# Optimization experiments

Measured on AMD Instinct MI355X. Metric: run time of the kernel, lower is better.

Reference implementation:

```python
import jax, jax.numpy as jnp
import numpy as np

B, S, D, H, DK = 32, 1024, 256, 8, 32
MASK_VALUE = -1e-30  # note: NOT -inf; masked scores become ~0 pre-softmax, faithful to source


def setup_inputs() -> dict:
    key = jax.random.key(0)
    ks = jax.random.split(key, 7)
    query = jax.random.normal(ks[0], (B, S, D), dtype=jnp.float32)
    key_t = jax.random.normal(ks[1], (B, S, D), dtype=jnp.float32)
    value = jax.random.normal(ks[2], (B, S, D), dtype=jnp.float32)
    # binary observation mask over key positions
    mask = (jax.random.uniform(ks[3], (B, S)) > 0.5).astype(jnp.float32)
    glorot = jax.nn.initializers.glorot_uniform(in_axis=1, out_axis=2)
    Wq = glorot(ks[4], (H, D, DK), jnp.float32)
    Wk = glorot(ks[5], (H, D, DK), jnp.float32)
    Wv = glorot(ks[6], (H, D, DK), jnp.float32)
    return {"query": query, "key": key_t, "value": value, "mask": mask,
            "Wq": Wq, "Wk": Wk, "Wv": Wv}


def reference(query, key, value, mask, Wq, Wk, Wv):
    # per-head projections, vectorized over heads: [B,S,D] x [H,D,DK] -> [B,H,S,DK]
    q = jnp.einsum('bsd,hdk->bhsk', query, Wq)
    k = jnp.einsum('bsd,hdk->bhsk', key, Wk)
    v = jnp.einsum('bsd,hdk->bhsk', value, Wv)
    # raw scores (no 1/sqrt(dk) scaling in source): [B,H,Sq,Sk]
    A = jnp.einsum('bhqk,bhsk->bhqs', q, k)
    m = mask[:, None, None, :]  # [B,1,1,Sk]
    A = m * A + (1.0 - m) * MASK_VALUE  # multiplicative mask, NOT additive
    A = jax.nn.softmax(A, axis=-1)
    out = jnp.einsum('bhqs,bhsk->bhqk', A, v)  # [B,H,Sq,DK]
    # concat heads along last dim, matching torch.cat order
    return out.transpose(0, 2, 1, 3).reshape(B, S, H * DK)
```

## Files before the change

### kernel.cpp

```cpp
#include <hip/hip_runtime.h>
#include <math.h>

#define B_  32
#define S_  1024
#define D_  256
#define H_  8
#define DK_ 32
#define MASKV (-1e-30f)
#define LOG2E 1.44269504f

typedef __attribute__((ext_vector_type(4))) short bf4_t;
typedef __attribute__((ext_vector_type(8))) short bf8_t;
typedef __attribute__((ext_vector_type(4))) float f4_t;

__device__ __forceinline__ unsigned fbits(float x) {
    union { float f; unsigned u; } v; v.f = x; return v.u;
}
__device__ __forceinline__ float bitsf(unsigned u) {
    union { unsigned u; float f; } v; v.u = u; return v.f;
}

#if __has_builtin(__builtin_amdgcn_exp2f)
#define EXP2F(x) __builtin_amdgcn_exp2f(x)
#else
#define EXP2F(x) __expf((x) * 0.69314718f)
#endif

__device__ __forceinline__ void gld16(const void* g, void* l) {
    __builtin_amdgcn_global_load_lds(
        (const __attribute__((address_space(1))) void*)g,
        (__attribute__((address_space(3))) void*)l, 16, 0, 0);
}

#define PSEL 0x07060302u

__global__ __launch_bounds__(256) void prep_w(
    const float* __restrict__ Wq, const float* __restrict__ Wk,
    const float* __restrict__ Wv, short* __restrict__ WtH, short* __restrict__ WtL)
{
    const int a = blockIdx.x >> 3;
    const int h = blockIdx.x & 7;
    const float* W = (a == 0 ? Wq : (a == 1 ? Wk : Wv)) + (size_t)h * 256 * 32;
    const int t = threadIdx.x;
    const int k    = t & 31;
    const int dgrp = t >> 5;
    short* th = WtH + ((size_t)a * 256 + h * 32 + k) * 256;
    short* tl = WtL + ((size_t)a * 256 + h * 32 + k) * 256;
#pragma unroll
    for (int jj = blockIdx.y * 2; jj < blockIdx.y * 2 + 2; ++jj) {
        const int d0 = jj * 32 + dgrp * 4;
        float x[4];
#pragma unroll
        for (int r = 0; r < 4; ++r) x[r] = W[(size_t)(d0 + r) * 32 + k];
        unsigned hu[4], lu[4];
#pragma unroll
        for (int r = 0; r < 4; ++r) {
            unsigned hb = (fbits(x[r]) + 0x8000u) & 0xFFFF0000u;
            hu[r] = hb;
            lu[r] = fbits(x[r] - bitsf(hb)) + 0x8000u;
        }
        uint2 hp = make_uint2(__builtin_amdgcn_perm(hu[1], hu[0], PSEL),
                              __builtin_amdgcn_perm(hu[3], hu[2], PSEL));
        uint2 lp = make_uint2(__builtin_amdgcn_perm(lu[1], lu[0], PSEL),
                              __builtin_amdgcn_perm(lu[3], lu[2], PSEL));
        *(uint2*)&th[d0] = hp;
        *(uint2*)&tl[d0] = lp;
    }
}

__global__ __launch_bounds__(256) void proj_kernel(
    const float* __restrict__ Xq, const float* __restrict__ Xk,
    const float* __restrict__ Xv, const float* __restrict__ mask,
    const short* __restrict__ WtH, const short* __restrict__ WtL,
    short* __restrict__ qpH, short* __restrict__ qpL,
    short* __restrict__ kpH, short* __restrict__ kpL,
    short* __restrict__ vpT)
{
    __shared__ __align__(16) short XsH[64 * 32];
    __shared__ __align__(16) short XsL[64 * 32];
    __shared__ __align__(16) short WsH[256 * 32];
    __shared__ __align__(16) short WsL[256 * 32];

    const int a  = blockIdx.y;
    const float* X = (a == 0 ? Xq : (a == 1 ? Xk : Xv));
    const short* WH = WtH + (size_t)a * 256 * 256;
    const short* WL = WtL + (size_t)a * 256 * 256;
    const int m0 = blockIdx.x * 64;

    const int tid  = threadIdx.x;
    const int lane = tid & 63;
    const int wv   = tid >> 6;
    const int l15  = lane & 15;
    const int quad = lane >> 4;

    f4_t acc[4][4];
#pragma unroll
    for (int i = 0; i < 4; ++i)
#pragma unroll
        for (int j = 0; j < 4; ++j) acc[i][j] = (f4_t){0.f, 0.f, 0.f, 0.f};

    for (int kc = 0; kc < 8; ++kc) {
        __syncthreads();
#pragma unroll
        for (int i = 0; i < 4; ++i) {
            size_t go = (size_t)((i * 4 + wv) * 16 + (lane >> 2)) * 256 + kc * 32 + (lane & 3) * 8;
            gld16(WH + go, (char*)WsH + (i * 4 + wv) * 1024);
            gld16(WL + go, (char*)WsL + (i * 4 + wv) * 1024);
        }
        {
            const float* xp = X + (size_t)(m0 + (tid >> 2)) * 256 + kc * 32 + (tid & 3) * 8;
            float4 x0 = *(const float4*)xp;
            float4 x1 = *(const float4*)(xp + 4);
            float xv[8] = {x0.x, x0.y, x0.z, x0.w, x1.x, x1.y, x1.z, x1.w};
            bf8_t hi, lo;
#pragma unroll
            for (int j = 0; j < 8; ++j) {
                unsigned hu = (fbits(xv[j]) + 0x8000u) & 0xFFFF0000u;
                hi[j] = (short)(hu >> 16);
                lo[j] = (short)((fbits(xv[j] - bitsf(hu)) + 0x8000u) >> 16);
            }
            *(bf8_t*)&XsH[(tid >> 2) * 32 + (tid & 3) * 8] = hi;
            *(bf8_t*)&XsL[(tid >> 2) * 32 + (tid & 3) * 8] = lo;
        }
        __syncthreads();

        bf8_t wH[4], wL[4];
#pragma unroll
        for (int ns = 0; ns < 4; ++ns) {
            int n = wv * 64 + ns * 16 + l15;
            wH[ns] = *(const bf8_t*)&WsH[n * 32 + quad * 8];
            wL[ns] = *(const bf8_t*)&WsL[n * 32 + quad * 8];
        }
#pragma unroll
        for (int t = 0; t < 4; ++t) {
            bf8_t xH = *(const bf8_t*)&XsH[(t * 16 + l15) * 32 + quad * 8];
            bf8_t xL = *(const bf8_t*)&XsL[(t * 16 + l15) * 32 + quad * 8];
#pragma unroll
            for (int ns = 0; ns < 4; ++ns) {
                f4_t c = acc[t][ns];
                if (a < 2) {
                    c = __builtin_amdgcn_mfma_f32_16x16x32_bf16(wH[ns], xH, c, 0, 0, 0);
                    c = __builtin_amdgcn_mfma_f32_16x16x32_bf16(wL[ns], xH, c, 0, 0, 0);
                    c = __builtin_amdgcn_mfma_f32_16x16x32_bf16(wH[ns], xL, c, 0, 0, 0);
                } else {
                    c = __builtin_amdgcn_mfma_f32_16x16x32_bf16(xH, wH[ns], c, 0, 0, 0);
                    c = __builtin_amdgcn_mfma_f32_16x16x32_bf16(xH, wL[ns], c, 0, 0, 0);
                    c = __builtin_amdgcn_mfma_f32_16x16x32_bf16(xL, wH[ns], c, 0, 0, 0);
                }
                acc[t][ns] = c;
            }
        }
    }

    const int b  = m0 >> 10;
    const int sB = m0 & 1023;
    if (a < 2) {
        short* dH = (a == 0) ? qpH : kpH;
        short* dL = (a == 0) ? qpL : kpL;
        const float* mbp = mask + (size_t)b * 1024;
#pragma unroll
        for (int t = 0; t < 4; ++t) {
            int s = sB + t * 16 + l15;
            const float scale = (a == 0) ? LOG2E : mbp[s];
#pragma unroll
            for (int ns = 0; ns < 4; ++ns) {
                int nw = wv * 64 + ns * 16 + quad * 4;
                int h = nw >> 5, k0 = nw & 31;
                unsigned hu[4], lu[4];
#pragma unroll
                for (int r = 0; r < 4; ++r) {
                    float x = acc[t][ns][r] * scale;
                    unsigned h32 = fbits(x) + 0x8000u;
                    hu[r] = h32;
                    float hf = bitsf(h32 & 0xFFFF0000u);
                    lu[r] = fbits(x - hf) + 0x8000u;
                }
                uint2 hp = make_uint2(__builtin_amdgcn_perm(hu[1], hu[0], PSEL),
                                      __builtin_amdgcn_perm(hu[3], hu[2], PSEL));
                uint2 lp = make_uint2(__builtin_amdgcn_perm(lu[1], lu[0], PSEL),
                                      __builtin_amdgcn_perm(lu[3], lu[2], PSEL));
                size_t off = ((size_t)(b * 8 + h) * 1024 + s) * 32 + k0;
                *(uint2*)&dH[off] = hp;
                *(uint2*)&dL[off] = lp;
            }
        }
    } else {
#pragma unroll
        for (int t = 0; t < 4; ++t) {
            int sr = sB + t * 16 + quad * 4;
#pragma unroll
            for (int ns = 0; ns < 4; ++ns) {
                int n = wv * 64 + ns * 16 + l15;
                int h = n >> 5, k = n & 31;
                unsigned eu[4];
#pragma unroll
                for (int r = 0; r < 4; ++r) eu[r] = fbits(acc[t][ns][r]) + 0x8000u;
                uint2 pk = make_uint2(__builtin_amdgcn_perm(eu[1], eu[0], PSEL),
                                      __builtin_amdgcn_perm(eu[3], eu[2], PSEL));
                *(uint2*)&vpT[((size_t)(b * 8 + h) * 32 + k) * 1024 + sr] = pk;
            }
        }
    }
}

__global__ __launch_bounds__(256) void attn_kernel(
    const short* __restrict__ qpH, const short* __restrict__ qpL,
    const short* __restrict__ kpH, const short* __restrict__ kpL,
    const short* __restrict__ vpT, float* __restrict__ out)
{
    __shared__ __align__(16) short KsH[2][64 * 32];
    __shared__ __align__(16) short KsL[2][64 * 32];
    __shared__ __align__(16) short VsT[2][32 * 72];

    const int tid  = threadIdx.x;
    const int lane = tid & 63;
    const int wv   = tid >> 6;
    const int l15  = lane & 15;
    const int quad = lane >> 4;

    const int L  = (blockIdx.z * gridDim.y + blockIdx.y) * gridDim.x + blockIdx.x;
    const int li = L >> 3;
    const int bh = (L & 7) * 32 + (li >> 3);
    const int qt = li & 7;
    const int b  = bh >> 3;
    const int h  = bh & 7;
    const int woff = qt * 128 + wv * 32;

    bf8_t qh[2], ql[2];
#pragma unroll
    for (int qs = 0; qs < 2; ++qs) {
        size_t row = (size_t)bh * 1024 + woff + qs * 16 + l15;
        qh[qs] = *(const bf8_t*)&qpH[row * 32 + quad * 8];
        ql[qs] = *(const bf8_t*)&qpL[row * 32 + quad * 8];
    }

    f4_t accO[2][2];
    f4_t accS[2];
#pragma unroll
    for (int i = 0; i < 2; ++i) {
        accS[i] = (f4_t){0.f, 0.f, 0.f, 0.f};
#pragma unroll
        for (int j = 0; j < 2; ++j) accO[i][j] = (f4_t){0.f, 0.f, 0.f, 0.f};
    }
    const bf4_t ones4 = {(short)0x3F80, (short)0x3F80, (short)0x3F80, (short)0x3F80};

    const int dv = tid >> 3, seg = tid & 7;

    {
        size_t toff = ((size_t)bh * 1024) * 32;
        gld16(kpH + toff + wv * 512 + lane * 8, (char*)KsH[0] + wv * 1024);
        gld16(kpL + toff + wv * 512 + lane * 8, (char*)KsL[0] + wv * 1024);
        uint4 v0 = *(const uint4*)&vpT[((size_t)bh * 32 + dv) * 1024 + seg * 8];
        *(uint4*)&VsT[0][dv * 72 + seg * 8] = v0;
    }
    __syncthreads();

    int cur = 0;
    for (int kt = 0; kt < 16; ++kt) {
        const int nxt = cur ^ 1;

        uint4 vreg;
        if (kt < 15) {
            size_t toff = ((size_t)bh * 1024 + (kt + 1) * 64) * 32;
            gld16(kpH + toff + wv * 512 + lane * 8, (char*)KsH[nxt] + wv * 1024);
            gld16(kpL + toff + wv * 512 + lane * 8, (char*)KsL[nxt] + wv * 1024);
            vreg = *(const uint4*)&vpT[((size_t)bh * 32 + dv) * 1024 + (kt + 1) * 64 + seg * 8];
        }

        f4_t sc[2][4];
#pragma unroll
        for (int ks = 0; ks < 4; ++ks) {
            bf8_t kh = *(const bf8_t*)&KsH[cur][(ks * 16 + l15) * 32 + quad * 8];
            bf8_t kl = *(const bf8_t*)&KsL[cur][(ks * 16 + l15) * 32 + quad * 8];
#pragma unroll
            for (int qs = 0; qs < 2; ++qs) {
                f4_t c = __builtin_amdgcn_mfma_f32_16x16x32_bf16(kh, qh[qs],
                             (f4_t){0.f, 0.f, 0.f, 0.f}, 0, 0, 0);
                c = __builtin_amdgcn_mfma_f32_16x16x32_bf16(kl, qh[qs], c, 0, 0, 0);
                c = __builtin_amdgcn_mfma_f32_16x16x32_bf16(kh, ql[qs], c, 0, 0, 0);
                sc[qs][ks] = c;
            }
        }

        bf4_t pf[2][4];
#pragma unroll
        for (int ks = 0; ks < 4; ++ks) {
#pragma unroll
            for (int qs = 0; qs < 2; ++qs) {
                unsigned eu[4];
#pragma unroll
                for (int r = 0; r < 4; ++r)
                    eu[r] = fbits(EXP2F(sc[qs][ks][r])) + 0x8000u;
                union { uint2 u; bf4_t v; } cv;
                cv.u = make_uint2(__builtin_amdgcn_perm(eu[1], eu[0], PSEL),
                                  __builtin_amdgcn_perm(eu[3], eu[2], PSEL));
                pf[qs][ks] = cv.v;
            }
        }

#pragma unroll
        for (int ks = 0; ks < 4; ++ks) {
            bf4_t vf0 = *(const bf4_t*)&VsT[cur][l15 * 72 + ks * 16 + quad * 4];
            bf4_t vf1 = *(const bf4_t*)&VsT[cur][(16 + l15) * 72 + ks * 16 + quad * 4];
#pragma unroll
            for (int qs = 0; qs < 2; ++qs) {
                accO[qs][0] = __builtin_amdgcn_mfma_f32_16x16x16bf16_1k(vf0, pf[qs][ks], accO[qs][0], 0, 0, 0);
                accO[qs][1] = __builtin_amdgcn_mfma_f32_16x16x16bf16_1k(vf1, pf[qs][ks], accO[qs][1], 0, 0, 0);
                accS[qs]    = __builtin_amdgcn_mfma_f32_16x16x16bf16_1k(ones4, pf[qs][ks], accS[qs], 0, 0, 0);
            }
        }

        if (kt < 15) *(uint4*)&VsT[nxt][dv * 72 + seg * 8] = vreg;
        __syncthreads();
        cur = nxt;
    }

#pragma unroll
    for (int qs = 0; qs < 2; ++qs) {
        float inv = 1.0f / accS[qs][0];
        int s = woff + qs * 16 + l15;
        float* op = out + ((size_t)b * 1024 + s) * 256 + h * 32;
#pragma unroll
        for (int dvs = 0; dvs < 2; ++dvs) {
            float4 o4 = make_float4(accO[qs][dvs][0] * inv, accO[qs][dvs][1] * inv,
                                    accO[qs][dvs][2] * inv, accO[qs][dvs][3] * inv);
            *(float4*)&op[dvs * 16 + quad * 4] = o4;
        }
    }
}

extern "C" void kernel_launch(void* const* d_in, const int* in_sizes, int n_in,
                              void* d_out, int out_size, void* d_ws, size_t ws_size,
                              hipStream_t stream)
{
    const float* query = (const float*)d_in[0];
    const float* key   = (const float*)d_in[1];
    const float* value = (const float*)d_in[2];
    const float* mask  = (const float*)d_in[3];
    const float* Wq    = (const float*)d_in[4];
    const float* Wk    = (const float*)d_in[5];
    const float* Wv    = (const float*)d_in[6];
    float* out = (float*)d_out;

    const size_t per = (size_t)B_ * H_ * S_ * DK_;
    short* qpH = (short*)d_ws;
    short* qpL = qpH + per;
    short* kpH = qpL + per;
    short* kpL = kpH + per;
    short* vpT = kpL + per;
    short* WtH = vpT + per;
    short* WtL = WtH + 3 * 256 * 256;

    prep_w<<<dim3(24, 4), 256, 0, stream>>>(Wq, Wk, Wv, WtH, WtL);
    proj_kernel<<<dim3(512, 3), 256, 0, stream>>>(query, key, value, mask, WtH, WtL,
                                                  qpH, qpL, kpH, kpL, vpT);
    attn_kernel<<<dim3(8, H_, B_), 256, 0, stream>>>(qpH, qpL, kpH, kpL, vpT, out);
}
```

Measured before the change: 279.0 us.

## Pre-swizzle weights and Q/K into MFMA fragment order, stage full X tile once

Weights and projected Q/K are now written directly in MFMA fragment-native layout, so each lane loads its 16-byte fragment with a contiguous access. The projection kernel loads weight fragments straight from global memory instead of staging them through LDS. It converts the whole 64x256 X tile into LDS once, cutting per-k-chunk barriers. The attention kernel reads K fragments from LDS without strided indexing and raises wave priority around the MFMA section. The trade-off is more LDS per block in the projection kernel (64KB), which may lower occupancy, and more global-memory traffic for weights.

```diff
diff --git a/kernel.cpp b/kernel.cpp
--- a/kernel.cpp
+++ b/kernel.cpp
@@ -34,9 +34,10 @@
 
 #define PSEL 0x07060302u
 
+
 __global__ __launch_bounds__(256) void prep_w(
     const float* __restrict__ Wq, const float* __restrict__ Wk,
-    const float* __restrict__ Wv, short* __restrict__ WtH, short* __restrict__ WtL)
+    const float* __restrict__ Wv, short* __restrict__ WpH, short* __restrict__ WpL)
 {
     const int a = blockIdx.x >> 3;
     const int h = blockIdx.x & 7;
@@ -44,8 +45,8 @@
     const int t = threadIdx.x;
     const int k    = t & 31;
     const int dgrp = t >> 5;
-    short* th = WtH + ((size_t)a * 256 + h * 32 + k) * 256;
-    short* tl = WtL + ((size_t)a * 256 + h * 32 + k) * 256;
+    const int ng   = h * 2 + (k >> 4);
+    const int l15  = k & 15;
 #pragma unroll
     for (int jj = blockIdx.y * 2; jj < blockIdx.y * 2 + 2; ++jj) {
         const int d0 = jj * 32 + dgrp * 4;
@@ -63,28 +64,30 @@
                               __builtin_amdgcn_perm(hu[3], hu[2], PSEL));
         uint2 lp = make_uint2(__builtin_amdgcn_perm(lu[1], lu[0], PSEL),
                               __builtin_amdgcn_perm(lu[3], lu[2], PSEL));
-        *(uint2*)&th[d0] = hp;
-        *(uint2*)&tl[d0] = lp;
+        const int quad = (d0 >> 3) & 3;
+        const int jb   = d0 & 7;
+        size_t off = (size_t)a * 65536
+                   + ((size_t)(jj * 16 + ng) * 64 + quad * 16 + l15) * 8 + jb;
+        *(uint2*)&WpH[off] = hp;
+        *(uint2*)&WpL[off] = lp;
     }
 }
 
 __global__ __launch_bounds__(256) void proj_kernel(
     const float* __restrict__ Xq, const float* __restrict__ Xk,
     const float* __restrict__ Xv, const float* __restrict__ mask,
-    const short* __restrict__ WtH, const short* __restrict__ WtL,
+    const short* __restrict__ WpH, const short* __restrict__ WpL,
     short* __restrict__ qpH, short* __restrict__ qpL,
     short* __restrict__ kpH, short* __restrict__ kpL,
     short* __restrict__ vpT)
 {
-    __shared__ __align__(16) short XsH[64 * 32];
-    __shared__ __align__(16) short XsL[64 * 32];
-    __shared__ __align__(16) short WsH[256 * 32];
-    __shared__ __align__(16) short WsL[256 * 32];
+    __shared__ __align__(16) short XsH[16384];
+    __shared__ __align__(16) short XsL[16384];
 
     const int a  = blockIdx.y;
     const float* X = (a == 0 ? Xq : (a == 1 ? Xk : Xv));
-    const short* WH = WtH + (size_t)a * 256 * 256;
-    const short* WL = WtL + (size_t)a * 256 * 256;
+    const short* WH = WpH + (size_t)a * 65536;
+    const short* WL = WpL + (size_t)a * 65536;
     const int m0 = blockIdx.x * 64;
 
     const int tid  = threadIdx.x;
@@ -93,59 +96,65 @@
     const int l15  = lane & 15;
     const int quad = lane >> 4;
 
+    {
+        const int r     = tid >> 2;
+        const int dhalf = tid & 3;
+        const int tix   = r >> 4;
+        const int rl15  = r & 15;
+        const float* xp = X + (size_t)(m0 + r) * 256 + dhalf * 64;
+#pragma unroll
+        for (int cc = 0; cc < 2; ++cc) {
+            const int kc = dhalf * 2 + cc;
+#pragma unroll
+            for (int q = 0; q < 4; ++q) {
+                float4 x0 = *(const float4*)(xp + cc * 32 + q * 8);
+                float4 x1 = *(const float4*)(xp + cc * 32 + q * 8 + 4);
+                float xv[8] = {x0.x, x0.y, x0.z, x0.w, x1.x, x1.y, x1.z, x1.w};
+                bf8_t hi, lo;
+#pragma unroll
+                for (int j = 0; j < 8; ++j) {
+                    unsigned hu = (fbits(xv[j]) + 0x8000u) & 0xFFFF0000u;
+                    hi[j] = (short)(hu >> 16);
+                    lo[j] = (short)((fbits(xv[j] - bitsf(hu)) + 0x8000u) >> 16);
+                }
+                const int off = ((kc * 4 + tix) * 64 + q * 16 + rl15) * 8;
+                *(bf8_t*)&XsH[off] = hi;
+                *(bf8_t*)&XsL[off] = lo;
+            }
+        }
+    }
+    __syncthreads();
+
     f4_t acc[4][4];
 #pragma unroll
     for (int i = 0; i < 4; ++i)
 #pragma unroll
         for (int j = 0; j < 4; ++j) acc[i][j] = (f4_t){0.f, 0.f, 0.f, 0.f};
 
+#pragma unroll
     for (int kc = 0; kc < 8; ++kc) {
-        __syncthreads();
-#pragma unroll
-        for (int i = 0; i < 4; ++i) {
-            size_t go = (size_t)((i * 4 + wv) * 16 + (lane >> 2)) * 256 + kc * 32 + (lane & 3) * 8;
-            gld16(WH + go, (char*)WsH + (i * 4 + wv) * 1024);
-            gld16(WL + go, (char*)WsL + (i * 4 + wv) * 1024);
-        }
-        {
-            const float* xp = X + (size_t)(m0 + (tid >> 2)) * 256 + kc * 32 + (tid & 3) * 8;
-            float4 x0 = *(const float4*)xp;
-            float4 x1 = *(const float4*)(xp + 4);
-            float xv[8] = {x0.x, x0.y, x0.z, x0.w, x1.x, x1.y, x1.z, x1.w};
-            bf8_t hi, lo;
-#pragma unroll
-            for (int j = 0; j < 8; ++j) {
-                unsigned hu = (fbits(xv[j]) + 0x8000u) & 0xFFFF0000u;
-                hi[j] = (short)(hu >> 16);
-                lo[j] = (short)((fbits(xv[j] - bitsf(hu)) + 0x8000u) >> 16);
-            }
-            *(bf8_t*)&XsH[(tid >> 2) * 32 + (tid & 3) * 8] = hi;
-            *(bf8_t*)&XsL[(tid >> 2) * 32 + (tid & 3) * 8] = lo;
-        }
-        __syncthreads();
-
-        bf8_t wH[4], wL[4];
+        bf8_t xH[4], xL[4];
+#pragma unroll
+        for (int t = 0; t < 4; ++t) {
+            xH[t] = *(const bf8_t*)&XsH[((kc * 4 + t) * 64 + lane) * 8];
+            xL[t] = *(const bf8_t*)&XsL[((kc * 4 + t) * 64 + lane) * 8];
+        }
 #pragma unroll
         for (int ns = 0; ns < 4; ++ns) {
-            int n = wv * 64 + ns * 16 + l15;
-            wH[ns] = *(const bf8_t*)&WsH[n * 32 + quad * 8];
-            wL[ns] = *(const bf8_t*)&WsL[n * 32 + quad * 8];
-        }
-#pragma unroll
-        for (int t = 0; t < 4; ++t) {
-            bf8_t xH = *(const bf8_t*)&XsH[(t * 16 + l15) * 32 + quad * 8];
-            bf8_t xL = *(const bf8_t*)&XsL[(t * 16 + l15) * 32 + quad * 8];
-#pragma unroll
-            for (int ns = 0; ns < 4; ++ns) {
+            const size_t wo = ((size_t)(kc * 16 + wv * 4 + ns) * 64 + lane) * 8;
+            bf8_t wh = *(const bf8_t*)&WH[wo];
+            bf8_t wl = *(const bf8_t*)&WL[wo];
+#pragma unroll
+            for (int t = 0; t < 4; ++t) {
                 f4_t c = acc[t][ns];
                 if (a < 2) {
-                    c = __builtin_amdgcn_mfma_f32_16x16x32_bf16(wH[ns], xH, c, 0, 0, 0);
-                    c = __builtin_amdgcn_mfma_f32_16x16x32_bf16(wL[ns], xH, c, 0, 0, 0);
-                    c = __builtin_amdgcn_mfma_f32_16x16x32_bf16(wH[ns], xL, c, 0, 0, 0);
+                    c = __builtin_amdgcn_mfma_f32_16x16x32_bf16(wh, xH[t], c, 0, 0, 0);
+                    c = __builtin_amdgcn_mfma_f32_16x16x32_bf16(wl, xH[t], c, 0, 0, 0);
+                    c = __builtin_amdgcn_mfma_f32_16x16x32_bf16(wh, xL[t], c, 0, 0, 0);
                 } else {
-                    c = __builtin_amdgcn_mfma_f32_16x16x32_bf16(xH, wH[ns], c, 0, 0, 0);
-                    c = __builtin_amdgcn_mfma_f32_16x16x32_bf16(xH, wL[ns], c, 0, 0, 0);
-                    c = __builtin_amdgcn_mfma_f32_16x16x32_bf16(xL, wH[ns], c, 0, 0, 0);
+                    c = __builtin_amdgcn_mfma_f32_16x16x32_bf16(xH[t], wh, c, 0, 0, 0);
+                    c = __builtin_amdgcn_mfma_f32_16x16x32_bf16(xH[t], wl, c, 0, 0, 0);
+                    c = __builtin_amdgcn_mfma_f32_16x16x32_bf16(xL[t], wh, c, 0, 0, 0);
                 }
                 acc[t][ns] = c;
             }
@@ -160,12 +169,14 @@
         const float* mbp = mask + (size_t)b * 1024;
 #pragma unroll
         for (int t = 0; t < 4; ++t) {
-            int s = sB + t * 16 + l15;
+            const int s = sB + t * 16 + l15;
             const float scale = (a == 0) ? LOG2E : mbp[s];
+            const int grp = (sB >> 4) + t;
 #pragma unroll
             for (int ns = 0; ns < 4; ++ns) {
-                int nw = wv * 64 + ns * 16 + quad * 4;
-                int h = nw >> 5, k0 = nw & 31;
+                const int h_    = wv * 2 + (ns >> 1);
+                const int quadA = (ns & 1) * 2 + (quad >> 1);
+                const int jb    = (quad & 1) * 4;
                 unsigned hu[4], lu[4];
 #pragma unroll
                 for (int r = 0; r < 4; ++r) {
@@ -179,7 +190,8 @@
                                       __builtin_amdgcn_perm(hu[3], hu[2], PSEL));
                 uint2 lp = make_uint2(__builtin_amdgcn_perm(lu[1], lu[0], PSEL),
                                       __builtin_amdgcn_perm(lu[3], lu[2], PSEL));
-                size_t off = ((size_t)(b * 8 + h) * 1024 + s) * 32 + k0;
+                size_t off = (((size_t)(b * 8 + h_) * 64 + grp) * 64
+                              + quadA * 16 + l15) * 8 + jb;
                 *(uint2*)&dH[off] = hp;
                 *(uint2*)&dL[off] = lp;
             }
@@ -208,8 +220,8 @@
     const short* __restrict__ kpH, const short* __restrict__ kpL,
     const short* __restrict__ vpT, float* __restrict__ out)
 {
-    __shared__ __align__(16) short KsH[2][64 * 32];
-    __shared__ __align__(16) short KsL[2][64 * 32];
+    __shared__ __align__(16) short KsH[2][2048];
+    __shared__ __align__(16) short KsL[2][2048];
     __shared__ __align__(16) short VsT[2][32 * 72];
 
     const int tid  = threadIdx.x;
@@ -229,9 +241,10 @@
     bf8_t qh[2], ql[2];
 #pragma unroll
     for (int qs = 0; qs < 2; ++qs) {
-        size_t row = (size_t)bh * 1024 + woff + qs * 16 + l15;
-        qh[qs] = *(const bf8_t*)&qpH[row * 32 + quad * 8];
-        ql[qs] = *(const bf8_t*)&qpL[row * 32 + quad * 8];
+        const int grp = qt * 8 + wv * 2 + qs;
+        size_t off = (((size_t)bh * 64 + grp) * 64 + lane) * 8;
+        qh[qs] = *(const bf8_t*)&qpH[off];
+        ql[qs] = *(const bf8_t*)&qpL[off];
     }
 
     f4_t accO[2][2];
@@ -247,7 +260,7 @@
     const int dv = tid >> 3, seg = tid & 7;
 
     {
-        size_t toff = ((size_t)bh * 1024) * 32;
+        size_t toff = ((size_t)bh * 64) * 512;
         gld16(kpH + toff + wv * 512 + lane * 8, (char*)KsH[0] + wv * 1024);
         gld16(kpL + toff + wv * 512 + lane * 8, (char*)KsL[0] + wv * 1024);
         uint4 v0 = *(const uint4*)&vpT[((size_t)bh * 32 + dv) * 1024 + seg * 8];
@@ -261,17 +274,18 @@
 
         uint4 vreg;
         if (kt < 15) {
-            size_t toff = ((size_t)bh * 1024 + (kt + 1) * 64) * 32;
+            size_t toff = ((size_t)bh * 64 + (kt + 1) * 4) * 512;
             gld16(kpH + toff + wv * 512 + lane * 8, (char*)KsH[nxt] + wv * 1024);
             gld16(kpL + toff + wv * 512 + lane * 8, (char*)KsL[nxt] + wv * 1024);
             vreg = *(const uint4*)&vpT[((size_t)bh * 32 + dv) * 1024 + (kt + 1) * 64 + seg * 8];
         }
 
+        __builtin_amdgcn_s_setprio(1);
         f4_t sc[2][4];
 #pragma unroll
         for (int ks = 0; ks < 4; ++ks) {
-            bf8_t kh = *(const bf8_t*)&KsH[cur][(ks * 16 + l15) * 32 + quad * 8];
-            bf8_t kl = *(const bf8_t*)&KsL[cur][(ks * 16 + l15) * 32 + quad * 8];
+            bf8_t kh = *(const bf8_t*)&KsH[cur][ks * 512 + lane * 8];
+            bf8_t kl = *(const bf8_t*)&KsL[cur][ks * 512 + lane * 8];
 #pragma unroll
             for (int qs = 0; qs < 2; ++qs) {
                 f4_t c = __builtin_amdgcn_mfma_f32_16x16x32_bf16(kh, qh[qs],
@@ -309,6 +323,7 @@
                 accS[qs]    = __builtin_amdgcn_mfma_f32_16x16x16bf16_1k(ones4, pf[qs][ks], accS[qs], 0, 0, 0);
             }
         }
+        __builtin_amdgcn_s_setprio(0);
 
         if (kt < 15) *(uint4*)&VsT[nxt][dv * 72 + seg * 8] = vreg;
         __syncthreads();
@@ -348,11 +363,11 @@
     short* kpH = qpL + per;
     short* kpL = kpH + per;
     short* vpT = kpL + per;
-    short* WtH = vpT + per;
-    short* WtL = WtH + 3 * 256 * 256;
-
-    prep_w<<<dim3(24, 4), 256, 0, stream>>>(Wq, Wk, Wv, WtH, WtL);
-    proj_kernel<<<dim3(512, 3), 256, 0, stream>>>(query, key, value, mask, WtH, WtL,
+    short* WpH = vpT + per;
+    short* WpL = WpH + 3 * 256 * 256;
+
+    prep_w<<<dim3(24, 4), 256, 0, stream>>>(Wq, Wk, Wv, WpH, WpL);
+    proj_kernel<<<dim3(512, 3), 256, 0, stream>>>(query, key, value, mask, WpH, WpL,
                                                   qpH, qpL, kpH, kpL, vpT);
     attn_kernel<<<dim3(8, H_, B_), 256, 0, stream>>>(qpH, qpL, kpH, kpL, vpT, out);
 }
```

Measured after the change: 277.6 us. Within noise of the previous version (-0.5%).
